# Performance work log

Hardware: AMD Instinct MI355X
Metric: run time of the kernel (lower is better)

Reference implementation:

```python
import jax, jax.numpy as jnp
import numpy as np

B = 256            # batch size
N_VARS = 8192      # variable nodes (LLR inputs)
N_CHECKS = 4096    # check nodes (zero-padded)
N_NODES = N_VARS + N_CHECKS
N_EDGES = 16_777_216
N_ITERS = 10       # num_iterations, unshared weights
NEG_SLOPE = 0.01   # F.leaky_relu default


def setup_inputs() -> dict:
    key = jax.random.key(0)
    ks = jax.random.split(key, 6)
    initial_llrs = jax.random.normal(ks[0], (B, N_VARS), dtype=jnp.float32)
    edge_index = jax.random.randint(ks[1], (2, N_EDGES), 0, B * N_NODES, dtype=jnp.int32)
    cycle_mask = jax.random.uniform(ks[2], (N_EDGES,), dtype=jnp.float32)
    # per-iteration layer params: Linear(3,1) weight/bias + scalars
    att_W = jax.random.normal(ks[3], (N_ITERS, 3), dtype=jnp.float32) * 0.5
    att_b = jax.random.normal(ks[4], (N_ITERS,), dtype=jnp.float32) * 0.1
    min_sum_scaler = jnp.full((N_ITERS,), 0.8, dtype=jnp.float32)
    cycle_penalty = jnp.full((N_ITERS,), -1.0, dtype=jnp.float32)
    return {
        "initial_llrs": initial_llrs,
        "edge_index": edge_index,
        "cycle_mask": cycle_mask,
        "att_W": att_W,
        "att_b": att_b,
        "min_sum_scaler": min_sum_scaler,
        "cycle_penalty": cycle_penalty,
    }


def reference(initial_llrs, edge_index, cycle_mask, att_W, att_b, min_sum_scaler, cycle_penalty):
    src, dst = edge_index[0], edge_index[1]
    # x0: [B, N_NODES] = LLRs padded with zeros for check nodes (residual each iter)
    x0 = jnp.concatenate(
        [initial_llrs, jnp.zeros((B, N_CHECKS), dtype=initial_llrs.dtype)], axis=1
    )

    def step(x, params):
        W, b, scaler, penalty = params  # W: [3], scalars otherwise
        xf = x.reshape(-1)             # [B*N_NODES]
        x_src = xf[src]                # [E] gather
        x_dst = xf[dst]                # [E] gather
        # Linear(3,1) over cat([x_src, x_dst, cycle_mask]) -> leaky_relu
        raw = x_src * W[0] + x_dst * W[1] + cycle_mask * W[2] + b
        raw = jnp.where(raw >= 0, raw, NEG_SLOPE * raw) + cycle_mask * penalty
        msgs = x_src * jax.nn.sigmoid(raw) * scaler   # [E]
        upd = jnp.zeros_like(xf).at[dst].add(msgs)    # scatter_add over flat nodes
        x_new = upd.reshape(B, N_NODES) + x0          # residual with initial LLRs
        return x_new, x_new[:, :N_VARS]

    _, outs = jax.lax.scan(
        step, x0, (att_W, att_b, min_sum_scaler, cycle_penalty)
    )
    return outs  # [N_ITERS, B, N_VARS] (stacked per-iteration variable LLRs)
```

## Files before the change

kernel.cpp:

```cpp
#include <hip/hip_runtime.h>

#define NV 8192
#define NC 4096
#define NN (NV + NC)
#define BATCH 256
#define TOT (BATCH * NN)
#define TOTP (TOT + 1024)
#define NEDGE 16777216
#define NITER 10
#define NBIN 3072
#define NPH 12
#define EPADF (NEDGE + NBIN * 256)
#define NB48 48
#define COARSECAP 393216
#define SCAP (NB48 * COARSECAP)
#define BINCAP 6144
#define PCK1 8192
#define CPAD2 16384
#define NCHK2 (COARSECAP / CPAD2)

typedef int   i4 __attribute__((ext_vector_type(4)));
typedef float f4 __attribute__((ext_vector_type(4)));
typedef unsigned int u32;
typedef unsigned short u16;
typedef u32 u4  __attribute__((ext_vector_type(4)));
typedef u16 us4 __attribute__((ext_vector_type(4)));

__global__ __launch_bounds__(256) void k_init(const float* __restrict__ llr,
                                              float* __restrict__ x) {
    int base = (blockIdx.x * 256 + threadIdx.x) * 4;
    if (base >= TOTP) return;
    f4 v = {0.f, 0.f, 0.f, 0.f};
    if (base < TOT) {
        int b = base / NN;
        int n = base - b * NN;
        if (n < NV) v = *reinterpret_cast<const f4*>(llr + (size_t)b * NV + n);
    }
    *reinterpret_cast<f4*>(x + base) = v;
}

__global__ void k_init48(int* __restrict__ cur48) {
    int t = threadIdx.x;
    if (t < NB48) cur48[t] = t * COARSECAP;
}

__global__ __launch_bounds__(256) void k_initb(int* __restrict__ cur3) {
    int b = blockIdx.x * 256 + threadIdx.x;
    if (b < NBIN) cur3[b] = b * BINCAP;
}

__global__ __launch_bounds__(256) void k_pass1(
    const int* __restrict__ src, const int* __restrict__ dst,
    const float* __restrict__ cm,
    u32* __restrict__ stg0, u16* __restrict__ stg1, int* __restrict__ cur48)
{
    __shared__ int wh[4][NB48];
    __shared__ int wcur[4][NB48];
    int t = threadIdx.x;
    int wv = t >> 6;
    for (int j = t; j < 4 * NB48; j += 256) ((int*)wh)[j] = 0;
    __syncthreads();
    int base = blockIdx.x * PCK1;
    for (int i = 0; i < PCK1; i += 1024) {
        i4 d = *reinterpret_cast<const i4*>(dst + base + i + t * 4);
        atomicAdd(&wh[wv][d.x >> 16], 1);
        atomicAdd(&wh[wv][d.y >> 16], 1);
        atomicAdd(&wh[wv][d.z >> 16], 1);
        atomicAdd(&wh[wv][d.w >> 16], 1);
    }
    __syncthreads();
    if (t < NB48) {
        int h0 = wh[0][t], h1 = wh[1][t], h2 = wh[2][t], h3 = wh[3][t];
        int tot = h0 + h1 + h2 + h3;
        int b0 = tot ? atomicAdd(&cur48[t], tot) : 0;
        wcur[0][t] = b0;
        wcur[1][t] = b0 + h0;
        wcur[2][t] = b0 + h0 + h1;
        wcur[3][t] = b0 + h0 + h1 + h2;
    }
    __syncthreads();
    for (int i = 0; i < PCK1; i += 1024) {
        i4 s4 = *reinterpret_cast<const i4*>(src + base + i + t * 4);
        i4 d4 = *reinterpret_cast<const i4*>(dst + base + i + t * 4);
        f4 c4 = *reinterpret_cast<const f4*>(cm + base + i + t * 4);
        int   ss[4] = {s4.x, s4.y, s4.z, s4.w};
        int   dd[4] = {d4.x, d4.y, d4.z, d4.w};
        float cc[4] = {c4.x, c4.y, c4.z, c4.w};
#pragma unroll
        for (int k = 0; k < 4; ++k) {
            int bkt = dd[k] >> 16;
            int pos = atomicAdd(&wcur[wv][bkt], 1);
            int q = (int)(cc[k] * 1024.0f + 0.5f);
            q = q > 1023 ? 1023 : q;
            stg0[pos] = ((u32)ss[k] << 10) | (u32)(dd[k] & 1023);
            stg1[pos] = (u16)((q << 6) | ((dd[k] >> 10) & 63));
        }
    }
}

__global__ __launch_bounds__(256) void k_pass2a(
    const u32* __restrict__ stg0, const u16* __restrict__ stg1,
    u32* __restrict__ iek, u16* __restrict__ iec,
    const int* __restrict__ cur48, int* __restrict__ cur3, int* __restrict__ cnt)
{
    __shared__ int lh[64 * NPH];
    __shared__ int lpos[64];
    int c = blockIdx.x / NCHK2;
    int k = blockIdx.x - c * NCHK2;
    int t = threadIdx.x;
    int cbase = c * COARSECAP;
    int vend = cur48[c];
    int start = cbase + k * CPAD2;
    int end = min(start + CPAD2, vend);
    if (start >= end) return;
    for (int j = t; j < 64 * NPH; j += 256) lh[j] = 0;
    __syncthreads();
    for (int i0 = start; i0 < end; i0 += 1024) {
        int i = i0 + t * 4;
        if (i + 4 <= end) {
            u4  w = *reinterpret_cast<const u4*>(stg0 + i);
            us4 v = *reinterpret_cast<const us4*>(stg1 + i);
            atomicAdd(&lh[(v.x & 63) * NPH + (w.x >> 28)], 1);
            atomicAdd(&lh[(v.y & 63) * NPH + (w.y >> 28)], 1);
            atomicAdd(&lh[(v.z & 63) * NPH + (w.z >> 28)], 1);
            atomicAdd(&lh[(v.w & 63) * NPH + (w.w >> 28)], 1);
        } else if (i < end) {
            for (int j = 0; j < end - i; ++j)
                atomicAdd(&lh[(stg1[i + j] & 63) * NPH + (stg0[i + j] >> 28)], 1);
        }
    }
    __syncthreads();
    if (t < 64) {
        int s = 0;
        for (int p = 0; p < NPH; ++p) s += lh[t * NPH + p];
        lpos[t] = s ? atomicAdd(&cur3[(c << 6) + t], s) : 0;
    }
    for (int j = t; j < 64 * NPH; j += 256)
        if (lh[j]) atomicAdd(&cnt[(c << 6) * NPH + j], lh[j]);
    __syncthreads();
    for (int i0 = start; i0 < end; i0 += 1024) {
        int i = i0 + t * 4;
        if (i + 4 <= end) {
            u4  w = *reinterpret_cast<const u4*>(stg0 + i);
            us4 v = *reinterpret_cast<const us4*>(stg1 + i);
            u32 ww[4] = {w.x, w.y, w.z, w.w};
            u16 vv[4] = {v.x, v.y, v.z, v.w};
#pragma unroll
            for (int j = 0; j < 4; ++j) {
                int pos = atomicAdd(&lpos[vv[j] & 63], 1);
                iek[pos] = ww[j];
                iec[pos] = (u16)(vv[j] >> 6);
            }
        } else if (i < end) {
            for (int j = 0; j < end - i; ++j) {
                u16 v1 = stg1[i + j];
                int pos = atomicAdd(&lpos[v1 & 63], 1);
                iek[pos] = stg0[i + j];
                iec[pos] = (u16)(v1 >> 6);
            }
        }
    }
}

__global__ __launch_bounds__(256) void k_scanp(
    const int* __restrict__ cnt, int* __restrict__ po)
{
    __shared__ int part[256];
    int t = threadIdx.x;
    int s = 0;
    for (int k = 0; k < 12; ++k) {
        int b = t * 12 + k;
        for (int p = 0; p < NPH; ++p) s += (cnt[b * NPH + p] + 3) & ~3;
    }
    part[t] = s;
    __syncthreads();
    for (int d = 1; d < 256; d <<= 1) {
        int v = (t >= d) ? part[t - d] : 0;
        __syncthreads();
        part[t] += v;
        __syncthreads();
    }
    int base = (t == 0) ? 0 : part[t - 1];
    for (int k = 0; k < 12; ++k) {
        int b = t * 12 + k;
        for (int p = 0; p < NPH; ++p) {
            po[b * 13 + p] = base;
            base += (cnt[b * NPH + p] + 3) & ~3;
        }
        po[b * 13 + 12] = base;
    }
}

__global__ __launch_bounds__(256) void k_pass2b(
    const u32* __restrict__ iek, const u16* __restrict__ iec,
    u32* __restrict__ fpk, u16* __restrict__ fcmh,
    const int* __restrict__ cnt, const int* __restrict__ po)
{
    __shared__ int lcur[NPH];
    __shared__ int lbt;
    int b = blockIdx.x;
    int t = threadIdx.x;
    if (t < NPH) lcur[t] = po[b * 13 + t];
    if (t == 0) {
        int s = 0;
        for (int p = 0; p < NPH; ++p) s += cnt[b * NPH + p];
        lbt = s;
    }
    __syncthreads();
    int s = b * BINCAP;
    int e = s + lbt;
    for (int i0 = s; i0 < e; i0 += 1024) {
        int i = i0 + t * 4;
        if (i + 4 <= e) {
            u4  w  = *reinterpret_cast<const u4*>(iek + i);
            us4 cq = *reinterpret_cast<const us4*>(iec + i);
            u32 ww[4] = {w.x, w.y, w.z, w.w};
            u16 cc[4] = {cq.x, cq.y, cq.z, cq.w};
#pragma unroll
            for (int j = 0; j < 4; ++j) {
                int p = (int)(ww[j] >> 28);
                int pos = atomicAdd(&lcur[p], 1);
                fpk[pos] = ww[j];
                fcmh[pos] = cc[j];
            }
        } else if (i < e) {
            for (int j = 0; j < e - i; ++j) {
                u32 w1 = iek[i + j];
                int p = (int)(w1 >> 28);
                int pos = atomicAdd(&lcur[p], 1);
                fpk[pos] = w1;
                fcmh[pos] = iec[i + j];
            }
        }
    }
    __syncthreads();
    if (t < NPH) {
        for (int j = lcur[t]; j < po[b * 13 + t + 1]; ++j) {
            fpk[j] = ((u32)TOT) << 10;
            fcmh[j] = 0;
        }
    }
}

__global__ __launch_bounds__(256) void k_iter2(
    const u32* __restrict__ fpk, const u16* __restrict__ fcmh,
    const int* __restrict__ po,
    const float* __restrict__ xin, float* __restrict__ xout,
    const float* __restrict__ llr, float* __restrict__ out,
    const float* __restrict__ attW, const float* __restrict__ attb,
    const float* __restrict__ scal, const float* __restrict__ pen, int it)
{
    const float W0 = attW[it * 3 + 0];
    const float W1 = attW[it * 3 + 1];
    const float W2 = attW[it * 3 + 2];
    const float bb = attb[it];
    const float sc = scal[it];
    const float pe = pen[it];
    const float QS = 1.0f / 1024.0f;

    __shared__ float acc[2048];
    __shared__ float xds[2048];
    int blk = blockIdx.x;
    int t = threadIdx.x;
    int b0 = blk << 1;
    int nbase = blk << 11;

    f4 z = {0.f, 0.f, 0.f, 0.f};
    *reinterpret_cast<f4*>(acc + t * 4) = z;
    *reinterpret_cast<f4*>(acc + 1024 + t * 4) = z;
    *reinterpret_cast<f4*>(xds + t * 4) =
        *reinterpret_cast<const f4*>(xin + nbase + t * 4);
    *reinterpret_cast<f4*>(xds + 1024 + t * 4) =
        *reinterpret_cast<const f4*>(xin + nbase + 1024 + t * 4);
    __syncthreads();

    int h = t >> 7;
    int tl = t & 127;
    int b = b0 + h;
    float* ac = acc + (h << 10);
    const float* xd = xds + (h << 10);
    const int* pob = po + b * 13;

    for (int p = 0; p < NPH; ++p) {
        int e = pob[p + 1];
        for (int i = pob[p] + tl * 4; i < e; i += 512) {
            u4  wa = *reinterpret_cast<const u4*>(fpk + i);
            us4 ca = *reinterpret_cast<const us4*>(fcmh + i);
            u32 w[4]  = {wa.x, wa.y, wa.z, wa.w};
            u16 cq[4] = {ca.x, ca.y, ca.z, ca.w};
            float xs[4];
#pragma unroll
            for (int k = 0; k < 4; ++k) xs[k] = xin[w[k] >> 10];
#pragma unroll
            for (int k = 0; k < 4; ++k) {
                int ldst = (int)(w[k] & 1023u);
                float cmv = (float)cq[k] * QS;
                float xdv = xd[ldst];
                float raw = fmaf(xs[k], W0, fmaf(xdv, W1, fmaf(cmv, W2, bb)));
                raw = (raw >= 0.f) ? raw : 0.01f * raw;
                raw = fmaf(cmv, pe, raw);
                float msg = xs[k] * sc / (1.0f + __expf(-raw));
                atomicAdd(ac + ldst, msg);
            }
        }
    }
    __syncthreads();

#pragma unroll
    for (int hh = 0; hh < 2; ++hh) {
        int bo = b0 + hh;
        int row = bo / 12, sub = bo - row * 12, n0 = sub << 10;
        f4 a = *reinterpret_cast<f4*>(acc + (hh << 10) + t * 4);
        if (n0 < NV) {
            f4 x0 = *reinterpret_cast<const f4*>(llr + (size_t)row * NV + n0 + t * 4);
            a += x0;
            __builtin_nontemporal_store(a,
                reinterpret_cast<f4*>(out + (size_t)it * (BATCH * NV) +
                                      (size_t)row * NV + n0 + t * 4));
        }
        *reinterpret_cast<f4*>(xout + (bo << 10) + t * 4) = a;
    }
}

__global__ __launch_bounds__(256) void k_edges(
    const int* __restrict__ src, const int* __restrict__ dst,
    const float* __restrict__ cm,
    const float* __restrict__ xin, float* __restrict__ xout,
    const float* __restrict__ attW, const float* __restrict__ attb,
    const float* __restrict__ scal, const float* __restrict__ pen, int it)
{
    const float W0 = attW[it * 3 + 0];
    const float W1 = attW[it * 3 + 1];
    const float W2 = attW[it * 3 + 2];
    const float bb = attb[it];
    const float sc = scal[it];
    const float pe = pen[it];
    int e = (blockIdx.x * 256 + threadIdx.x) * 4;
    i4 s4 = *reinterpret_cast<const i4*>(src + e);
    i4 d4 = *reinterpret_cast<const i4*>(dst + e);
    f4 c4 = *reinterpret_cast<const f4*>(cm + e);
    int   si[4] = {s4.x, s4.y, s4.z, s4.w};
    int   di[4] = {d4.x, d4.y, d4.z, d4.w};
    float cc[4] = {c4.x, c4.y, c4.z, c4.w};
#pragma unroll
    for (int k = 0; k < 4; ++k) {
        float xs = xin[si[k]];
        float xd = xin[di[k]];
        float raw = fmaf(xs, W0, fmaf(xd, W1, fmaf(cc[k], W2, bb)));
        raw = (raw >= 0.f) ? raw : 0.01f * raw;
        raw = fmaf(cc[k], pe, raw);
        float sig = 1.0f / (1.0f + __expf(-raw));
        atomicAdd(xout + di[k], xs * sig * sc);
    }
}

__global__ __launch_bounds__(256) void k_emit_init(
    const float* __restrict__ xnew, const float* __restrict__ llr,
    float* __restrict__ xother, float* __restrict__ out, int it)
{
    int base = (blockIdx.x * 256 + threadIdx.x) * 4;
    if (base >= TOTP) return;
    f4 z = {0.f, 0.f, 0.f, 0.f};
    if (base < TOT) {
        int b = base / NN;
        int n = base - b * NN;
        if (n < NV) {
            f4 v = *reinterpret_cast<const f4*>(xnew + base);
            *reinterpret_cast<f4*>(out + (size_t)it * (BATCH * NV) +
                                   (size_t)b * NV + n) = v;
            *reinterpret_cast<f4*>(xother + base) =
                *reinterpret_cast<const f4*>(llr + (size_t)b * NV + n);
        } else {
            *reinterpret_cast<f4*>(xother + base) = z;
        }
    } else {
        *reinterpret_cast<f4*>(xother + base) = z;
    }
}

extern "C" void kernel_launch(void* const* d_in, const int* in_sizes, int n_in,
                              void* d_out, int out_size, void* d_ws, size_t ws_size,
                              hipStream_t stream) {
    const float* llr  = (const float*)d_in[0];
    const int*   ei   = (const int*)d_in[1];
    const float* cm   = (const float*)d_in[2];
    const float* attW = (const float*)d_in[3];
    const float* attb = (const float*)d_in[4];
    const float* scal = (const float*)d_in[5];
    const float* pen  = (const float*)d_in[6];
    float* out = (float*)d_out;
    const int* src = ei;
    const int* dst = ei + NEDGE;

    char* w = (char*)d_ws;
    u32* iek = (u32*)w;                         w += (size_t)SCAP * 4;
    u16* iec = (u16*)w;                         w += (((size_t)SCAP * 2 + 15) & ~15ull);
    char* reg2 = w;
    u32* stg0 = (u32*)reg2;
    u16* stg1 = (u16*)(reg2 + (size_t)SCAP * 4);
    u32* fpk  = (u32*)reg2;
    u16* fcmh = (u16*)(reg2 + (size_t)EPADF * 4);
    w += (size_t)SCAP * 4 + (((size_t)SCAP * 2 + 15) & ~15ull);
    int* cnt   = (int*)w;                       w += (size_t)NBIN * NPH * 4;
    int* po    = (int*)w;                       w += (size_t)NBIN * 13 * 4;
    int* cur3  = (int*)w;                       w += (size_t)NBIN * 4;
    int* cur48 = (int*)w;                       w += (size_t)NB48 * 4;
    size_t need = (size_t)(w - (char*)d_ws);

    float* xA = (float*)iek;
    float* xB = xA + TOTP;

    dim3 blk(256);
    dim3 gNode((TOTP / 4 + 255) / 256);

    if (ws_size >= need) {
        hipMemsetAsync(cnt, 0, (size_t)NBIN * NPH * sizeof(int), stream);
        k_init48<<<1, 64, 0, stream>>>(cur48);
        k_initb<<<(NBIN + 255) / 256, blk, 0, stream>>>(cur3);
        k_pass1<<<NEDGE / PCK1, blk, 0, stream>>>(src, dst, cm, stg0, stg1, cur48);
        k_pass2a<<<NB48 * NCHK2, blk, 0, stream>>>(stg0, stg1, iek, iec, cur48, cur3, cnt);
        k_scanp<<<1, blk, 0, stream>>>(cnt, po);
        k_pass2b<<<NBIN, blk, 0, stream>>>(iek, iec, fpk, fcmh, cnt, po);

        k_init<<<gNode, blk, 0, stream>>>(llr, xA);
        k_init<<<gNode, blk, 0, stream>>>(llr, xB);
        for (int it = 0; it < NITER; ++it) {
            k_iter2<<<NBIN / 2, blk, 0, stream>>>(fpk, fcmh, po, xA, xB, llr, out,
                                                  attW, attb, scal, pen, it);
            float* tswp = xA; xA = xB; xB = tswp;
        }
    } else {
        float* fA = (float*)d_ws;
        float* fB = fA + TOTP;
        k_init<<<gNode, blk, 0, stream>>>(llr, fA);
        k_init<<<gNode, blk, 0, stream>>>(llr, fB);
        for (int it = 0; it < NITER; ++it) {
            k_edges<<<NEDGE / 4 / 256, blk, 0, stream>>>(src, dst, cm, fA, fB,
                                                         attW, attb, scal, pen, it);
            k_emit_init<<<gNode, blk, 0, stream>>>(fB, llr, fA, out, it);
            float* tswp = fA; fA = fB; fB = tswp;
        }
    }
}
```

Baseline: 1.562 ms.

## Process both bins with full block per phase, simplify pass1 histogram, enlarge chunks

The per-iteration gather kernel now has all 256 threads work on each of the two bins in turn, one phase at a time, instead of splitting the block into two 128-thread halves with one bin each. This is meant to balance load when the two bins differ in edge count, at the cost of a bounds check per iteration. The one-time pass1 binning drops its per-wave histograms for a single shared histogram, which brings more LDS atomic contention. The pass1 and pass2 chunk sizes are doubled.

Measured after the change: 1.340 ms. 14.2% less time.

```diff
diff --git a/kernel.cpp b/kernel.cpp
--- a/kernel.cpp
+++ b/kernel.cpp
@@ -15,8 +15,8 @@
 #define COARSECAP 393216
 #define SCAP (NB48 * COARSECAP)
 #define BINCAP 6144
-#define PCK1 8192
-#define CPAD2 16384
+#define PCK1 16384
+#define CPAD2 32768
 #define NCHK2 (COARSECAP / CPAD2)
 
 typedef int   i4 __attribute__((ext_vector_type(4)));
@@ -54,29 +54,22 @@
     const float* __restrict__ cm,
     u32* __restrict__ stg0, u16* __restrict__ stg1, int* __restrict__ cur48)
 {
-    __shared__ int wh[4][NB48];
-    __shared__ int wcur[4][NB48];
-    int t = threadIdx.x;
-    int wv = t >> 6;
-    for (int j = t; j < 4 * NB48; j += 256) ((int*)wh)[j] = 0;
+    __shared__ int lh[NB48], lpos[NB48];
+    int t = threadIdx.x;
+    if (t < NB48) lh[t] = 0;
     __syncthreads();
     int base = blockIdx.x * PCK1;
     for (int i = 0; i < PCK1; i += 1024) {
         i4 d = *reinterpret_cast<const i4*>(dst + base + i + t * 4);
-        atomicAdd(&wh[wv][d.x >> 16], 1);
-        atomicAdd(&wh[wv][d.y >> 16], 1);
-        atomicAdd(&wh[wv][d.z >> 16], 1);
-        atomicAdd(&wh[wv][d.w >> 16], 1);
+        atomicAdd(&lh[d.x >> 16], 1);
+        atomicAdd(&lh[d.y >> 16], 1);
+        atomicAdd(&lh[d.z >> 16], 1);
+        atomicAdd(&lh[d.w >> 16], 1);
     }
     __syncthreads();
     if (t < NB48) {
-        int h0 = wh[0][t], h1 = wh[1][t], h2 = wh[2][t], h3 = wh[3][t];
-        int tot = h0 + h1 + h2 + h3;
-        int b0 = tot ? atomicAdd(&cur48[t], tot) : 0;
-        wcur[0][t] = b0;
-        wcur[1][t] = b0 + h0;
-        wcur[2][t] = b0 + h0 + h1;
-        wcur[3][t] = b0 + h0 + h1 + h2;
+        int c = lh[t];
+        lpos[t] = c ? atomicAdd(&cur48[t], c) : 0;
     }
     __syncthreads();
     for (int i = 0; i < PCK1; i += 1024) {
@@ -89,7 +82,7 @@
 #pragma unroll
         for (int k = 0; k < 4; ++k) {
             int bkt = dd[k] >> 16;
-            int pos = atomicAdd(&wcur[wv][bkt], 1);
+            int pos = atomicAdd(&lpos[bkt], 1);
             int q = (int)(cc[k] * 1024.0f + 0.5f);
             q = q > 1023 ? 1023 : q;
             stg0[pos] = ((u32)ss[k] << 10) | (u32)(dd[k] & 1023);
@@ -274,43 +267,45 @@
         *reinterpret_cast<const f4*>(xin + nbase + 1024 + t * 4);
     __syncthreads();
 
-    int h = t >> 7;
-    int tl = t & 127;
-    int b = b0 + h;
-    float* ac = acc + (h << 10);
-    const float* xd = xds + (h << 10);
-    const int* pob = po + b * 13;
-
     for (int p = 0; p < NPH; ++p) {
-        int e = pob[p + 1];
-        for (int i = pob[p] + tl * 4; i < e; i += 512) {
-            u4  wa = *reinterpret_cast<const u4*>(fpk + i);
-            us4 ca = *reinterpret_cast<const us4*>(fcmh + i);
-            u32 w[4]  = {wa.x, wa.y, wa.z, wa.w};
-            u16 cq[4] = {ca.x, ca.y, ca.z, ca.w};
-            float xs[4];
-#pragma unroll
-            for (int k = 0; k < 4; ++k) xs[k] = xin[w[k] >> 10];
-#pragma unroll
-            for (int k = 0; k < 4; ++k) {
-                int ldst = (int)(w[k] & 1023u);
-                float cmv = (float)cq[k] * QS;
-                float xdv = xd[ldst];
-                float raw = fmaf(xs[k], W0, fmaf(xdv, W1, fmaf(cmv, W2, bb)));
-                raw = (raw >= 0.f) ? raw : 0.01f * raw;
-                raw = fmaf(cmv, pe, raw);
-                float msg = xs[k] * sc / (1.0f + __expf(-raw));
-                atomicAdd(ac + ldst, msg);
+#pragma unroll
+        for (int h = 0; h < 2; ++h) {
+            int b = b0 + h;
+            int s = po[b * 13 + p], e = po[b * 13 + p + 1];
+            float* ac = acc + (h << 10);
+            const float* xd = xds + (h << 10);
+            for (int i0 = s; i0 < e; i0 += 1024) {
+                int i = i0 + t * 4;
+                if (i < e) {
+                    u4  wa = *reinterpret_cast<const u4*>(fpk + i);
+                    us4 ca = *reinterpret_cast<const us4*>(fcmh + i);
+                    u32 w[4]  = {wa.x, wa.y, wa.z, wa.w};
+                    u16 cq[4] = {ca.x, ca.y, ca.z, ca.w};
+                    float xs[4];
+#pragma unroll
+                    for (int k = 0; k < 4; ++k) xs[k] = xin[w[k] >> 10];
+#pragma unroll
+                    for (int k = 0; k < 4; ++k) {
+                        int ldst = (int)(w[k] & 1023u);
+                        float cmv = (float)cq[k] * QS;
+                        float xdv = xd[ldst];
+                        float raw = fmaf(xs[k], W0, fmaf(xdv, W1, fmaf(cmv, W2, bb)));
+                        raw = (raw >= 0.f) ? raw : 0.01f * raw;
+                        raw = fmaf(cmv, pe, raw);
+                        float msg = xs[k] * sc / (1.0f + __expf(-raw));
+                        atomicAdd(ac + ldst, msg);
+                    }
+                }
             }
         }
     }
     __syncthreads();
 
 #pragma unroll
-    for (int hh = 0; hh < 2; ++hh) {
-        int bo = b0 + hh;
-        int row = bo / 12, sub = bo - row * 12, n0 = sub << 10;
-        f4 a = *reinterpret_cast<f4*>(acc + (hh << 10) + t * 4);
+    for (int h = 0; h < 2; ++h) {
+        int b = b0 + h;
+        int row = b / 12, sub = b - row * 12, n0 = sub << 10;
+        f4 a = *reinterpret_cast<f4*>(acc + (h << 10) + t * 4);
         if (n0 < NV) {
             f4 x0 = *reinterpret_cast<const f4*>(llr + (size_t)row * NV + n0 + t * 4);
             a += x0;
@@ -318,7 +313,7 @@
                 reinterpret_cast<f4*>(out + (size_t)it * (BATCH * NV) +
                                       (size_t)row * NV + n0 + t * 4));
         }
-        *reinterpret_cast<f4*>(xout + (bo << 10) + t * 4) = a;
+        *reinterpret_cast<f4*>(xout + (b << 10) + t * 4) = a;
     }
 }
 
```
